# Optimization experiments

Measured on AMD Instinct MI355X. Metric: run time of the kernel, lower is better.

The kernel has to match this reference:

```python
import jax, jax.numpy as jnp
import numpy as np


def fwht(x):
    """Fast Walsh-Hadamard transform over last axis (power-of-2 length), normalized by 1/sqrt(n).
    Matches matmul_hadU with K=1 (pure Hadamard rotation)."""
    orig_shape = x.shape
    n = orig_shape[-1]
    x = x.reshape(-1, n)
    h = 1
    while h < n:
        x = x.reshape(-1, n // (2 * h), 2, h)
        a = x[:, :, 0, :]
        b = x[:, :, 1, :]
        x = jnp.stack([a + b, a - b], axis=2)
        h *= 2
    x = x.reshape(orig_shape)
    return x * (1.0 / np.sqrt(n)).astype(np.float32)


def setup_inputs() -> dict:
    key = jax.random.key(0)
    k1, k2, k3, k4, k5 = jax.random.split(key, 5)
    B, S, n, m = 2, 2048, 4096, 4096
    CODEBOOK = 65536  # 2^16 E8P codes, each decoding an 8-dim lattice point
    inp = jax.random.normal(k1, (B, S, n), dtype=jnp.float32)
    # SU/SV are random sign-like diagonal rescales in QuIP; use unit-variance floats here
    SU = jax.random.normal(k2, (n,), dtype=jnp.float32)
    SV = jax.random.normal(k3, (m,), dtype=jnp.float32)
    grid = jax.random.normal(k4, (CODEBOOK, 8), dtype=jnp.float32) * 0.1
    Qidxs = jax.random.randint(k5, (m, n // 8), 0, CODEBOOK, dtype=jnp.int32)
    return {"input": inp, "SU": SU, "SV": SV, "grid": grid, "Qidxs": Qidxs}


def reference(input, SU, SV, grid, Qidxs):
    n = SU.shape[0]
    m = SV.shape[0]
    x = input.reshape(-1, n) * SU          # diagonal rescale by SU
    x = fwht(x)                             # left Hadamard rotation
    # Dequantize packed E8P codebook: each 16-bit code -> 8 weights
    W = grid[Qidxs].reshape(m, n)           # [m, n]
    x = x @ W.T                             # dense GEMM against dequantized weight
    x = fwht(x)                             # right Hadamard rotation
    x = x * SV                              # diagonal rescale by SV
    return x.reshape(input.shape[:-1] + (m,))
```

## Files before the change

kernel.cpp:

```cpp
#include <hip/hip_runtime.h>
#include <stdint.h>

typedef __bf16 bf16x8 __attribute__((ext_vector_type(8)));
typedef float f32x4 __attribute__((ext_vector_type(4)));

__device__ __forceinline__ unsigned int f2bf(float f) {
  unsigned int u = __float_as_uint(f);
  return (u + 0x7fffu + ((u >> 16) & 1u)) >> 16;
}
__device__ __forceinline__ unsigned int pack2(float a, float b) {
  return f2bf(a) | (f2bf(b) << 16);
}

__device__ __forceinline__ void fwht16(float v[16]) {
#pragma unroll
  for (int s = 0; s < 4; ++s) {
    const int h = 1 << s;
#pragma unroll
    for (int i = 0; i < 16; ++i) {
      if (!(i & h)) {
        float a = v[i], b = v[i ^ h];
        v[i] = a + b;
        v[i ^ h] = a - b;
      }
    }
  }
}

#define LP(i) ((i) + ((i) >> 5))

__global__ void __launch_bounds__(256) k_fwht_in(const float* __restrict__ X,
                                                 const float* __restrict__ SU,
                                                 unsigned short* __restrict__ Xh) {
  __shared__ float lds[4224];
  const int t = threadIdx.x;
  const size_t row = blockIdx.x;
  const float4* xr = (const float4*)(X + row * 4096);
  const float4* su = (const float4*)SU;
  float v[16];
#pragma unroll
  for (int q = 0; q < 4; ++q) {
    float4 a = xr[4 * t + q], s = su[4 * t + q];
    v[4 * q + 0] = a.x * s.x;
    v[4 * q + 1] = a.y * s.y;
    v[4 * q + 2] = a.z * s.z;
    v[4 * q + 3] = a.w * s.w;
  }
  fwht16(v);
#pragma unroll
  for (int q = 0; q < 4; ++q) {
    int i0 = 16 * t + 4 * q;
    *(float4*)&lds[LP(i0)] = make_float4(v[4 * q], v[4 * q + 1], v[4 * q + 2], v[4 * q + 3]);
  }
  __syncthreads();
  const int b = ((t >> 4) << 8) | (t & 15);
#pragma unroll
  for (int j = 0; j < 16; ++j) { int i = b + 16 * j; v[j] = lds[LP(i)]; }
  fwht16(v);
#pragma unroll
  for (int j = 0; j < 16; ++j) { int i = b + 16 * j; lds[LP(i)] = v[j]; }
  __syncthreads();
#pragma unroll
  for (int j = 0; j < 16; ++j) { int i = t + 256 * j; v[j] = lds[LP(i)]; }
  fwht16(v);
  unsigned short* orow = Xh + row * 4096;
#pragma unroll
  for (int j = 0; j < 16; ++j)
    orow[t + 256 * j] = (unsigned short)f2bf(v[j] * 0.015625f);
}

__global__ void __launch_bounds__(256) k_decompress(const int* __restrict__ Qidxs,
                                                    const float* __restrict__ G,
                                                    unsigned short* __restrict__ Wh) {
  int e = blockIdx.x * 256 + threadIdx.x;
  int idx = Qidxs[e];
  const float4* g = (const float4*)(G + (size_t)idx * 8);
  float4 a = g[0], b = g[1];
  uint4 o;
  o.x = pack2(a.x, a.y);
  o.y = pack2(a.z, a.w);
  o.z = pack2(b.x, b.y);
  o.w = pack2(b.z, b.w);
  ((uint4*)Wh)[e] = o;
}

__device__ __forceinline__ void gl2lds16(const unsigned short* g, unsigned short* l) {
  __builtin_amdgcn_global_load_lds(
      (const __attribute__((address_space(1))) void*)g,
      (__attribute__((address_space(3))) void*)l, 16, 0, 0);
}

__global__ void __launch_bounds__(256) k_gemm_bt(const unsigned short* __restrict__ A,
                                                 const unsigned short* __restrict__ B,
                                                 float* __restrict__ C) {
  const int K = 4096, N = 4096;
  __shared__ unsigned short sA[128 * 64];
  __shared__ unsigned short sB[128 * 64];
  const int tid = threadIdx.x;
  const int wave = tid >> 6, lane = tid & 63;
  const int bn = blockIdx.x, bm = blockIdx.y;
  const int wr = wave >> 1, wc = wave & 1;
  const int frow = lane & 15;
  const int sw = frow & 7;
  const int jbase = lane >> 4;
  f32x4 acc[4][4] = {};

  const size_t rowA0 = (size_t)bm * 128;
  const size_t rowB0 = (size_t)bn * 128;

  for (int kt = 0; kt < K; kt += 64) {
    __syncthreads();
#pragma unroll
    for (int it = 0; it < 4; ++it) {
      int c = it * 256 + tid;
      int r = c >> 3;
      int jg = (c & 7) ^ (r & 7);
      int kc = jg * 8;
      unsigned short* la = &sA[(it * 256 + wave * 64) * 8];
      unsigned short* lb = &sB[(it * 256 + wave * 64) * 8];
      gl2lds16(A + (rowA0 + r) * K + kt + kc, la);
      gl2lds16(B + (rowB0 + r) * K + kt + kc, lb);
    }
    __syncthreads();
#pragma unroll
    for (int kk = 0; kk < 64; kk += 32) {
      bf16x8 af[4], bfr[4];
      int jn = (kk >> 3) + jbase;
      int js = jn ^ sw;
#pragma unroll
      for (int i = 0; i < 4; ++i)
        af[i] = *(const bf16x8*)&sA[(wr * 64 + i * 16 + frow) * 64 + js * 8];
#pragma unroll
      for (int j = 0; j < 4; ++j)
        bfr[j] = *(const bf16x8*)&sB[(wc * 64 + j * 16 + frow) * 64 + js * 8];
#pragma unroll
      for (int i = 0; i < 4; ++i)
#pragma unroll
        for (int j = 0; j < 4; ++j)
          acc[i][j] = __builtin_amdgcn_mfma_f32_16x16x32_bf16(af[i], bfr[j], acc[i][j], 0, 0, 0);
    }
  }
  const int crow = bm * 128 + wr * 64 + (lane >> 4) * 4;
  const int ccol = bn * 128 + wc * 64 + (lane & 15);
#pragma unroll
  for (int i = 0; i < 4; ++i)
#pragma unroll
    for (int j = 0; j < 4; ++j) {
      float* cp = C + (size_t)(crow + i * 16) * N + ccol + j * 16;
#pragma unroll
      for (int r = 0; r < 4; ++r) cp[(size_t)r * N] = acc[i][j][r];
    }
}

__global__ void __launch_bounds__(256) k_fwht_out(float* __restrict__ Y,
                                                  const float* __restrict__ SV) {
  __shared__ float lds[4224];
  const int t = threadIdx.x;
  const size_t row = blockIdx.x;
  float* yrow = Y + row * 4096;
  const float4* yr = (const float4*)yrow;
  float v[16];
#pragma unroll
  for (int q = 0; q < 4; ++q) {
    float4 a = yr[4 * t + q];
    v[4 * q + 0] = a.x;
    v[4 * q + 1] = a.y;
    v[4 * q + 2] = a.z;
    v[4 * q + 3] = a.w;
  }
  fwht16(v);
#pragma unroll
  for (int q = 0; q < 4; ++q) {
    int i0 = 16 * t + 4 * q;
    *(float4*)&lds[LP(i0)] = make_float4(v[4 * q], v[4 * q + 1], v[4 * q + 2], v[4 * q + 3]);
  }
  __syncthreads();
  const int b = ((t >> 4) << 8) | (t & 15);
#pragma unroll
  for (int j = 0; j < 16; ++j) { int i = b + 16 * j; v[j] = lds[LP(i)]; }
  fwht16(v);
#pragma unroll
  for (int j = 0; j < 16; ++j) { int i = b + 16 * j; lds[LP(i)] = v[j]; }
  __syncthreads();
#pragma unroll
  for (int j = 0; j < 16; ++j) { int i = t + 256 * j; v[j] = lds[LP(i)]; }
  fwht16(v);
#pragma unroll
  for (int j = 0; j < 16; ++j) {
    int i = t + 256 * j;
    yrow[i] = v[j] * SV[i] * 0.015625f;
  }
}

extern "C" void kernel_launch(void* const* d_in, const int* in_sizes, int n_in,
                              void* d_out, int out_size, void* d_ws, size_t ws_size,
                              hipStream_t stream) {
  const float* X     = (const float*)d_in[0];
  const float* SU    = (const float*)d_in[1];
  const float* SV    = (const float*)d_in[2];
  const float* G     = (const float*)d_in[3];
  const int*   Qidxs = (const int*)d_in[4];
  float* out = (float*)d_out;

  unsigned short* Xh = (unsigned short*)d_ws;
  unsigned short* Wh = Xh + (size_t)4096 * 4096;

  k_fwht_in<<<4096, 256, 0, stream>>>(X, SU, Xh);
  k_decompress<<<(4096 * 512) / 256, 256, 0, stream>>>(Qidxs, G, Wh);
  k_gemm_bt<<<dim3(32, 32), 256, 0, stream>>>(Xh, Wh, out);
  k_fwht_out<<<4096, 256, 0, stream>>>(out, SV);
}
```

Baseline: 318.3 us.

## Rewrite GEMM as 256x256 tile, 8-wave, double-buffered pipelined kernel

The bf16 GEMM moves from 128x128 tiles with 4 waves to 256x256 tiles with 8 waves. Global-to-LDS loads for the next k-tile are interleaved with MFMA phases using explicit barriers, waitcnt, sched_barrier and setprio. Larger tiles raise data reuse per load, and the software pipeline hides load latency behind compute. In exchange the kernel uses much more LDS and many more accumulator registers, and the hand-written synchronisation is fragile. Only 256 blocks are launched, which may underfill the GPU.

```diff
diff --git a/kernel.cpp b/kernel.cpp
--- a/kernel.cpp
+++ b/kernel.cpp
@@ -90,65 +90,111 @@
       (__attribute__((address_space(3))) void*)l, 16, 0, 0);
 }
 
-__global__ void __launch_bounds__(256) k_gemm_bt(const unsigned short* __restrict__ A,
-                                                 const unsigned short* __restrict__ B,
-                                                 float* __restrict__ C) {
+#define BARX() __builtin_amdgcn_s_barrier()
+#define SCHEDB() __builtin_amdgcn_sched_barrier(0)
+#define WAITL0() asm volatile("s_waitcnt lgkmcnt(0)" ::: "memory")
+#define WAITV4() asm volatile("s_waitcnt vmcnt(4)" ::: "memory")
+
+#define APHASE(q, STMT, TAIL)                                                   \
+  {                                                                             \
+    bf16x8 af[2][2];                                                            \
+    _Pragma("unroll") for (int mm = 0; mm < 2; ++mm)                            \
+        _Pragma("unroll") for (int kh = 0; kh < 2; ++kh)                        \
+            af[mm][kh] = *(const bf16x8*)&sAp[((wr << 7) + (((q)*2 + mm) << 4) + frow) * 64 + \
+                                              ((((kh << 2) + jb) ^ sw) << 3)];  \
+    STMT;                                                                       \
+    BARX();                                                                     \
+    WAITL0();                                                                   \
+    SCHEDB();                                                                   \
+    __builtin_amdgcn_s_setprio(1);                                              \
+    _Pragma("unroll") for (int mm = 0; mm < 2; ++mm)                            \
+        _Pragma("unroll") for (int n = 0; n < 4; ++n)                           \
+            _Pragma("unroll") for (int kh = 0; kh < 2; ++kh)                    \
+                acc[(q)*2 + mm][n] = __builtin_amdgcn_mfma_f32_16x16x32_bf16(   \
+                    af[mm][kh], bq[n][kh], acc[(q)*2 + mm][n], 0, 0, 0);        \
+    __builtin_amdgcn_s_setprio(0);                                              \
+    TAIL;                                                                       \
+    BARX();                                                                     \
+    SCHEDB();                                                                   \
+  }
+
+__global__ void __launch_bounds__(512, 2)
+k_gemm_bt(const unsigned short* __restrict__ A,
+          const unsigned short* __restrict__ B,
+          float* __restrict__ C) {
   const int K = 4096, N = 4096;
-  __shared__ unsigned short sA[128 * 64];
-  __shared__ unsigned short sB[128 * 64];
+  __shared__ unsigned short sA[2][256 * 64];
+  __shared__ unsigned short sB[2][256 * 64];
   const int tid = threadIdx.x;
-  const int wave = tid >> 6, lane = tid & 63;
+  const int lane = tid & 63;
+  const int wave = tid >> 6;
+  const int wr = wave >> 2;
+  const int wc = wave & 3;
+  const int frow = lane & 15;
+  const int jb = lane >> 4;
+  const int sw = frow & 7;
   const int bn = blockIdx.x, bm = blockIdx.y;
-  const int wr = wave >> 1, wc = wave & 1;
-  const int frow = lane & 15;
-  const int sw = frow & 7;
-  const int jbase = lane >> 4;
-  f32x4 acc[4][4] = {};
-
-  const size_t rowA0 = (size_t)bm * 128;
-  const size_t rowB0 = (size_t)bn * 128;
-
-  for (int kt = 0; kt < K; kt += 64) {
-    __syncthreads();
-#pragma unroll
-    for (int it = 0; it < 4; ++it) {
-      int c = it * 256 + tid;
-      int r = c >> 3;
-      int jg = (c & 7) ^ (r & 7);
-      int kc = jg * 8;
-      unsigned short* la = &sA[(it * 256 + wave * 64) * 8];
-      unsigned short* lb = &sB[(it * 256 + wave * 64) * 8];
-      gl2lds16(A + (rowA0 + r) * K + kt + kc, la);
-      gl2lds16(B + (rowB0 + r) * K + kt + kc, lb);
+  const size_t rowA0 = (size_t)bm * 256;
+  const size_t rowB0 = (size_t)bn * 256;
+
+  f32x4 acc[8][4] = {};
+
+  auto stage = [&](const unsigned short* __restrict__ G, size_t row0,
+                   unsigned short* dst, int h, int ktile) {
+    const int kt = (ktile < 64 ? ktile : 0) << 6;
+#pragma unroll
+    for (int l = 0; l < 2; ++l) {
+      const int c = (l << 9) + tid;
+      const int r = c >> 3;
+      const int jg = (c & 7) ^ (r & 7);
+      gl2lds16(G + (row0 + (size_t)((h << 7) + r)) * K + kt + (jg << 3),
+               dst + (h << 13) + (c << 3));
     }
-    __syncthreads();
-#pragma unroll
-    for (int kk = 0; kk < 64; kk += 32) {
-      bf16x8 af[4], bfr[4];
-      int jn = (kk >> 3) + jbase;
-      int js = jn ^ sw;
-#pragma unroll
-      for (int i = 0; i < 4; ++i)
-        af[i] = *(const bf16x8*)&sA[(wr * 64 + i * 16 + frow) * 64 + js * 8];
-#pragma unroll
-      for (int j = 0; j < 4; ++j)
-        bfr[j] = *(const bf16x8*)&sB[(wc * 64 + j * 16 + frow) * 64 + js * 8];
-#pragma unroll
-      for (int i = 0; i < 4; ++i)
-#pragma unroll
-        for (int j = 0; j < 4; ++j)
-          acc[i][j] = __builtin_amdgcn_mfma_f32_16x16x32_bf16(af[i], bfr[j], acc[i][j], 0, 0, 0);
-    }
-  }
-  const int crow = bm * 128 + wr * 64 + (lane >> 4) * 4;
-  const int ccol = bn * 128 + wc * 64 + (lane & 15);
-#pragma unroll
-  for (int i = 0; i < 4; ++i)
-#pragma unroll
-    for (int j = 0; j < 4; ++j) {
-      float* cp = C + (size_t)(crow + i * 16) * N + ccol + j * 16;
-#pragma unroll
-      for (int r = 0; r < 4; ++r) cp[(size_t)r * N] = acc[i][j][r];
+  };
+
+  auto group = [&](int p, int gA, int gB) {
+    const unsigned short* sAp = sA[p];
+    const unsigned short* sBp = sB[p];
+    unsigned short* sAn = sA[p ^ 1];
+    unsigned short* sBn = sB[p];
+    bf16x8 bq[4][2];
+#pragma unroll
+    for (int n = 0; n < 4; ++n)
+#pragma unroll
+      for (int kh = 0; kh < 2; ++kh)
+        bq[n][kh] = *(const bf16x8*)&sBp[((wc << 6) + (n << 4) + frow) * 64 +
+                                         ((((kh << 2) + jb) ^ sw) << 3)];
+    APHASE(0, (stage(A, rowA0, sAn, 0, gA)), ((void)0));
+    APHASE(1, (stage(A, rowA0, sAn, 1, gA)), ((void)0));
+    APHASE(2, (stage(B, rowB0, sBn, 0, gB)), ((void)0));
+    APHASE(3, (stage(B, rowB0, sBn, 1, gB)), WAITV4());
+  };
+
+  stage(B, rowB0, sB[0], 0, 0);
+  stage(B, rowB0, sB[0], 1, 0);
+  stage(A, rowA0, sA[0], 0, 0);
+  stage(A, rowA0, sA[0], 1, 0);
+  stage(B, rowB0, sB[1], 0, 1);
+  stage(B, rowB0, sB[1], 1, 1);
+  WAITV4();
+  BARX();
+  SCHEDB();
+
+#pragma unroll 1
+  for (int i = 0; i < 32; ++i) {
+    group(0, 2 * i + 1, 2 * i + 2);
+    group(1, 2 * i + 2, 2 * i + 3);
+  }
+
+  const int rbase = bm * 256 + (wr << 7) + (jb << 2);
+  const int cbase = bn * 256 + (wc << 6) + frow;
+#pragma unroll
+  for (int m = 0; m < 8; ++m)
+#pragma unroll
+    for (int n = 0; n < 4; ++n) {
+      float* cp = C + (size_t)(rbase + (m << 4)) * N + cbase + (n << 4);
+#pragma unroll
+      for (int r = 0; r < 4; ++r) cp[(size_t)r * N] = acc[m][n][r];
     }
 }
 
@@ -207,6 +253,6 @@
 
   k_fwht_in<<<4096, 256, 0, stream>>>(X, SU, Xh);
   k_decompress<<<(4096 * 512) / 256, 256, 0, stream>>>(Qidxs, G, Wh);
-  k_gemm_bt<<<dim3(32, 32), 256, 0, stream>>>(Xh, Wh, out);
+  k_gemm_bt<<<dim3(16, 16), 512, 0, stream>>>(Xh, Wh, out);
   k_fwht_out<<<4096, 256, 0, stream>>>(out, SV);
 }
```

Result: faster. 280.4 us (-11.9%).
